# Optimization experiments

Hardware: AMD Instinct MI355X
Metric: run time of the kernel (lower is better)

Reference implementation:

```python
import jax, jax.numpy as jnp
import numpy as np

N_HEADS = 8
D_KV = 64
NUM_BUCKETS = 32
MAX_DISTANCE = 128


def _relative_position_bucket(relative_position, bidirectional=True,
                              num_buckets=NUM_BUCKETS, max_distance=MAX_DISTANCE):
    # Faithful port of T5Attention._relative_position_bucket (bidirectional path).
    n = -relative_position
    if bidirectional:
        num_buckets //= 2
        ret = (n < 0).astype(jnp.int32) * num_buckets
        n = jnp.abs(n)
    else:
        ret = jnp.zeros_like(n)
        n = jnp.maximum(n, 0)
    max_exact = num_buckets // 2
    is_small = n < max_exact
    val_if_large = max_exact + (
        jnp.log(n.astype(jnp.float32) / max_exact)
        / np.log(max_distance / max_exact)
        * (num_buckets - max_exact)
    ).astype(jnp.int32)
    val_if_large = jnp.minimum(val_if_large, num_buckets - 1)
    return ret + jnp.where(is_small, n, val_if_large)


def setup_inputs() -> dict:
    key = jax.random.key(0)
    ks = jax.random.split(key, 6)
    bs, qlen, d_model = 2, 2048, 512
    inner = N_HEADS * D_KV
    s = 1.0 / np.sqrt(d_model)
    return {
        "input": jax.random.normal(ks[0], (bs, qlen, d_model), jnp.float32),
        "Wq": jax.random.normal(ks[1], (d_model, inner), jnp.float32) * s,
        "Wk": jax.random.normal(ks[2], (d_model, inner), jnp.float32) * s,
        "Wv": jax.random.normal(ks[3], (d_model, inner), jnp.float32) * s,
        "Wo": jax.random.normal(ks[4], (inner, d_model), jnp.float32) * s,
        "rel_bias": jax.random.normal(ks[5], (NUM_BUCKETS, N_HEADS), jnp.float32),
    }


def reference(input, Wq, Wk, Wv, Wo, rel_bias):
    bs, qlen, d_model = input.shape

    def shape(x):  # [b, s, inner] -> [b, h, s, d]
        return x.reshape(bs, qlen, N_HEADS, D_KV).transpose(0, 2, 1, 3)

    q = shape(input @ Wq)
    k = shape(input @ Wk)
    v = shape(input @ Wv)

    # Raw scores (T5: no 1/sqrt(d) scaling)
    scores = jnp.einsum("bhqd,bhkd->bhqk", q, k)

    # Relative position bias: bucket [q, k] -> [h, q, k]
    pos = jnp.arange(qlen)
    rel_pos = pos[None, :] - pos[:, None]  # memory - query
    buckets = _relative_position_bucket(rel_pos, bidirectional=True)
    position_bias = rel_bias[buckets].transpose(2, 0, 1)[None]  # [1, h, q, k]

    scores = scores + position_bias
    weights = jax.nn.softmax(scores.astype(jnp.float32), axis=-1).astype(scores.dtype)

    context = jnp.einsum("bhqk,bhkd->bhqd", weights, v)
    context = context.transpose(0, 2, 1, 3).reshape(bs, qlen, N_HEADS * D_KV)
    return context @ Wo
```

## Files before the change

### kernel.cpp

```cpp
#include <hip/hip_runtime.h>
#include <hip/hip_bf16.h>
#include <cmath>

typedef __bf16 bf16_t;
typedef __bf16 bf16x8 __attribute__((ext_vector_type(8)));
typedef __bf16 bf16x4 __attribute__((ext_vector_type(4)));
typedef float f32x4 __attribute__((ext_vector_type(4)));

#define QLEN 2048
#define DMODEL 512
#define NH 8
#define DKV 64
#define INNER 512
#define LOG2E 1.44269504f
#define THR_LOG2 11.5415603f

__global__ __launch_bounds__(256) void cvt_split(const float* __restrict__ in,
                                                 bf16_t* __restrict__ hi,
                                                 bf16_t* __restrict__ lo, int n4) {
  int i = blockIdx.x * 256 + threadIdx.x;
  if (i >= n4) return;
  float4 v = reinterpret_cast<const float4*>(in)[i];
  bf16x4 h, l;
  #pragma unroll
  for (int j = 0; j < 4; ++j) {
    float x = (&v.x)[j];
    bf16_t hb = (bf16_t)x;
    h[j] = hb;
    l[j] = (bf16_t)(x - (float)hb);
  }
  reinterpret_cast<bf16x4*>(hi)[i] = h;
  reinterpret_cast<bf16x4*>(lo)[i] = l;
}

__global__ __launch_bounds__(256) void transpose512_split_all(
    const float* __restrict__ W0, const float* __restrict__ W1,
    const float* __restrict__ W2, const float* __restrict__ W3,
    bf16_t* __restrict__ H0, bf16_t* __restrict__ L0,
    bf16_t* __restrict__ H1, bf16_t* __restrict__ L1,
    bf16_t* __restrict__ H2, bf16_t* __restrict__ L2,
    bf16_t* __restrict__ H3, bf16_t* __restrict__ L3) {
  __shared__ float tile[32][33];
  int z = blockIdx.z;
  const float* W = z == 0 ? W0 : z == 1 ? W1 : z == 2 ? W2 : W3;
  bf16_t* Whi    = z == 0 ? H0 : z == 1 ? H1 : z == 2 ? H2 : H3;
  bf16_t* Wlo    = z == 0 ? L0 : z == 1 ? L1 : z == 2 ? L2 : L3;
  int bk = blockIdx.x * 32, bn = blockIdx.y * 32;
  int tx = threadIdx.x, ty = threadIdx.y;
  #pragma unroll
  for (int i = 0; i < 32; i += 8)
    tile[ty + i][tx] = W[(size_t)(bk + ty + i) * DMODEL + bn + tx];
  __syncthreads();
  #pragma unroll
  for (int i = 0; i < 32; i += 8) {
    float v = tile[tx][ty + i];
    bf16_t hb = (bf16_t)v;
    size_t o = (size_t)(bn + ty + i) * DMODEL + bk + tx;
    Whi[o] = hb;
    Wlo[o] = (bf16_t)(v - (float)hb);
  }
}

#define GST 68
template<int MODE>
__global__ __launch_bounds__(256) void gemm64(const bf16_t* __restrict__ A,
                                              const bf16_t* __restrict__ Bt,
                                              bf16_t* __restrict__ Cb,
                                              float* __restrict__ Cf) {
  __shared__ bf16_t sA[64 * GST];
  __shared__ bf16_t sB[64 * GST];
  const int m0 = blockIdx.x * 64, n0 = blockIdx.y * 64;
  const int tid = threadIdx.x;
  const int lane = tid & 63, w = tid >> 6;
  const int wr = (w >> 1) * 32, wc = (w & 1) * 32;
  const int l16 = lane & 15, lg = lane >> 4;

  f32x4 acc[2][2] = {};

  for (int k0 = 0; k0 < DMODEL; k0 += 64) {
    #pragma unroll
    for (int i = 0; i < 2; ++i) {
      int chunk = tid + i * 256;
      int row = chunk >> 3, c8 = (chunk & 7) * 8;
      *reinterpret_cast<bf16x8*>(&sA[row * GST + c8]) =
          *reinterpret_cast<const bf16x8*>(&A[(size_t)(m0 + row) * DMODEL + k0 + c8]);
      *reinterpret_cast<bf16x8*>(&sB[row * GST + c8]) =
          *reinterpret_cast<const bf16x8*>(&Bt[(size_t)(n0 + row) * DMODEL + k0 + c8]);
    }
    __syncthreads();
    #pragma unroll
    for (int ks = 0; ks < 2; ++ks) {
      bf16x8 af[2], bfr[2];
      #pragma unroll
      for (int i = 0; i < 2; ++i)
        af[i] = *reinterpret_cast<const bf16x8*>(&sA[(wr + i * 16 + l16) * GST + ks * 32 + lg * 8]);
      #pragma unroll
      for (int j = 0; j < 2; ++j)
        bfr[j] = *reinterpret_cast<const bf16x8*>(&sB[(wc + j * 16 + l16) * GST + ks * 32 + lg * 8]);
      #pragma unroll
      for (int i = 0; i < 2; ++i)
        #pragma unroll
        for (int j = 0; j < 2; ++j)
          acc[i][j] = __builtin_amdgcn_mfma_f32_16x16x32_bf16(af[i], bfr[j], acc[i][j], 0, 0, 0);
    }
    __syncthreads();
  }

  #pragma unroll
  for (int i = 0; i < 2; ++i)
    #pragma unroll
    for (int j = 0; j < 2; ++j)
      #pragma unroll
      for (int r = 0; r < 4; ++r) {
        int m = m0 + wr + i * 16 + lg * 4 + r;
        int n = n0 + wc + j * 16 + l16;
        float v = acc[i][j][r];
        if (MODE == 1) {
          int b = m >> 11, s = m & (QLEN - 1);
          Cb[(size_t)(b * INNER + n) * QLEN + s] = (bf16_t)v;
        } else {
          Cf[(size_t)m * DMODEL + n] = v;
        }
      }
}

__global__ __launch_bounds__(256) void gemm_qk_split(const bf16_t* __restrict__ Ah,
                                                     const bf16_t* __restrict__ Al,
                                                     const bf16_t* __restrict__ Bqh,
                                                     const bf16_t* __restrict__ Bql,
                                                     const bf16_t* __restrict__ Bkh,
                                                     const bf16_t* __restrict__ Bkl,
                                                     bf16_t* __restrict__ Qh,
                                                     bf16_t* __restrict__ Ql,
                                                     bf16_t* __restrict__ Kh,
                                                     bf16_t* __restrict__ Kl) {
  __shared__ bf16_t sAh[64 * GST];
  __shared__ bf16_t sAl[64 * GST];
  __shared__ bf16_t sBh[128 * GST];
  __shared__ bf16_t sBl[128 * GST];
  const int m0 = blockIdx.x * 64;
  const int n0g = blockIdx.y * 128;
  const bool isK = n0g >= 512;
  const int n0 = n0g & 511;
  const bf16_t* __restrict__ Bh = isK ? Bkh : Bqh;
  const bf16_t* __restrict__ Bl = isK ? Bkl : Bql;
  bf16_t* __restrict__ Ch = isK ? Kh : Qh;
  bf16_t* __restrict__ Cl = isK ? Kl : Ql;

  const int tid = threadIdx.x;
  const int lane = tid & 63, w = tid >> 6;
  const int wr = (w >> 1) * 32, wc = (w & 1) * 64;
  const int l16 = lane & 15, lg = lane >> 4;

  f32x4 acc[2][4] = {};

  for (int k0 = 0; k0 < DMODEL; k0 += 64) {
    #pragma unroll
    for (int i = 0; i < 2; ++i) {
      int chunk = tid + i * 256;
      int row = chunk >> 3, c8 = (chunk & 7) * 8;
      size_t ga = (size_t)(m0 + row) * DMODEL + k0 + c8;
      *reinterpret_cast<bf16x8*>(&sAh[row * GST + c8]) = *reinterpret_cast<const bf16x8*>(&Ah[ga]);
      *reinterpret_cast<bf16x8*>(&sAl[row * GST + c8]) = *reinterpret_cast<const bf16x8*>(&Al[ga]);
    }
    #pragma unroll
    for (int i = 0; i < 4; ++i) {
      int chunk = tid + i * 256;
      int row = chunk >> 3, c8 = (chunk & 7) * 8;
      size_t gb = (size_t)(n0 + row) * DMODEL + k0 + c8;
      *reinterpret_cast<bf16x8*>(&sBh[row * GST + c8]) = *reinterpret_cast<const bf16x8*>(&Bh[gb]);
      *reinterpret_cast<bf16x8*>(&sBl[row * GST + c8]) = *reinterpret_cast<const bf16x8*>(&Bl[gb]);
    }
    __syncthreads();
    #pragma unroll
    for (int ks = 0; ks < 2; ++ks) {
      bf16x8 ah[2], al[2], bh[4], bl[4];
      #pragma unroll
      for (int i = 0; i < 2; ++i) {
        int ro = (wr + i * 16 + l16) * GST + ks * 32 + lg * 8;
        ah[i] = *reinterpret_cast<const bf16x8*>(&sAh[ro]);
        al[i] = *reinterpret_cast<const bf16x8*>(&sAl[ro]);
      }
      #pragma unroll
      for (int j = 0; j < 4; ++j) {
        int ro = (wc + j * 16 + l16) * GST + ks * 32 + lg * 8;
        bh[j] = *reinterpret_cast<const bf16x8*>(&sBh[ro]);
        bl[j] = *reinterpret_cast<const bf16x8*>(&sBl[ro]);
      }
      #pragma unroll
      for (int i = 0; i < 2; ++i)
        #pragma unroll
        for (int j = 0; j < 4; ++j) {
          acc[i][j] = __builtin_amdgcn_mfma_f32_16x16x32_bf16(ah[i], bh[j], acc[i][j], 0, 0, 0);
          acc[i][j] = __builtin_amdgcn_mfma_f32_16x16x32_bf16(ah[i], bl[j], acc[i][j], 0, 0, 0);
          acc[i][j] = __builtin_amdgcn_mfma_f32_16x16x32_bf16(al[i], bh[j], acc[i][j], 0, 0, 0);
        }
    }
    __syncthreads();
  }

  #pragma unroll
  for (int i = 0; i < 2; ++i)
    #pragma unroll
    for (int j = 0; j < 4; ++j)
      #pragma unroll
      for (int r = 0; r < 4; ++r) {
        int m = m0 + wr + i * 16 + lg * 4 + r;
        int n = n0 + wc + j * 16 + l16;
        float v = acc[i][j][r];
        if (!isK) v *= LOG2E;
        bf16_t hb = (bf16_t)v;
        size_t o = (size_t)m * INNER + n;
        Ch[o] = hb;
        if (!isK) Cl[o] = (bf16_t)(v - (float)hb);
      }
}

__device__ __forceinline__ float redmax16(float v) {
  v = fmaxf(v, __shfl_xor(v, 1));
  v = fmaxf(v, __shfl_xor(v, 2));
  v = fmaxf(v, __shfl_xor(v, 4));
  v = fmaxf(v, __shfl_xor(v, 8));
  return v;
}
__device__ __forceinline__ float redsum16(float v) {
  v += __shfl_xor(v, 1);
  v += __shfl_xor(v, 2);
  v += __shfl_xor(v, 4);
  v += __shfl_xor(v, 8);
  return v;
}
__device__ __forceinline__ int t5_bucket_abs(int n) {
  if (n < 8)  return n;
  if (n < 12) return 8;
  if (n < 16) return 9;
  if (n < 23) return 10;
  if (n < 32) return 11;
  if (n < 46) return 12;
  if (n < 64) return 13;
  if (n < 91) return 14;
  return 15;
}

#define SKS 68
#define SVS 132
#define SPS 66

struct StageRegs { bf16x8 kh[2], v[2]; };

__device__ __forceinline__ void stage_load(StageRegs& r, const bf16_t* __restrict__ Kh,
                                           const bf16_t* __restrict__ Vt,
                                           int b, int h, int k0, int tid) {
  #pragma unroll
  for (int i = 0; i < 2; ++i) {
    int chunk = tid + i * 512;
    int krow = chunk >> 3, kc8 = (chunk & 7) * 8;
    int vrow = chunk >> 4, vc8 = (chunk & 15) * 8;
    r.kh[i] = *reinterpret_cast<const bf16x8*>(
        &Kh[(size_t)(b * QLEN + k0 + krow) * INNER + h * DKV + kc8]);
    r.v[i] = *reinterpret_cast<const bf16x8*>(
        &Vt[(size_t)((b * NH + h) * DKV + vrow) * QLEN + k0 + vc8]);
  }
}
__device__ __forceinline__ void stage_write(const StageRegs& r, bf16_t* dKh, bf16_t* dV,
                                            int tid) {
  #pragma unroll
  for (int i = 0; i < 2; ++i) {
    int chunk = tid + i * 512;
    int krow = chunk >> 3, kc8 = (chunk & 7) * 8;
    int vrow = chunk >> 4, vc8 = (chunk & 15) * 8;
    *reinterpret_cast<bf16x8*>(&dKh[krow * SKS + kc8]) = r.kh[i];
    *reinterpret_cast<bf16x8*>(&dV [vrow * SVS + vc8]) = r.v[i];
  }
}

__global__ __launch_bounds__(512, 4) void attn_kernel(const bf16_t* __restrict__ Qh,
                                                      const bf16_t* __restrict__ Ql,
                                                      const bf16_t* __restrict__ Kh,
                                                      const bf16_t* __restrict__ Vt,
                                                      const float* __restrict__ relb,
                                                      bf16_t* __restrict__ ctx) {
  __shared__ bf16_t sKh[128 * SKS];
  __shared__ bf16_t sV [64 * SVS];
  __shared__ bf16_t sP [2][64 * SPS];
  __shared__ float sM[2][64], sL[2][64];
  __shared__ float sBiasH[32];
  float* sAcc = (float*)&sP[0][0];

  const int id = blockIdx.x;
  const int lin = (id & 7) * 64 + (id >> 3);
  const int qt = lin & 31, h = (lin >> 5) & 7, b = lin >> 8;

  const int tid = threadIdx.x, lane = tid & 63, w = tid >> 6;
  const int l16 = lane & 15, lg = lane >> 4;
  const int q0 = qt * 64;
  const int qg = w & 3, half = w >> 2;
  const int wq = qg * 16;
  const int kh0 = half * 64;

  if (tid < 32) sBiasH[tid] = relb[tid * NH + h] * LOG2E;

  bf16x8 qh[2], ql[2];
  #pragma unroll
  for (int ks = 0; ks < 2; ++ks) {
    size_t o = (size_t)(b * QLEN + q0 + wq + l16) * INNER + h * DKV + ks * 32 + lg * 8;
    qh[ks] = *reinterpret_cast<const bf16x8*>(&Qh[o]);
    ql[ks] = *reinterpret_cast<const bf16x8*>(&Ql[o]);
  }

  f32x4 acc[4] = {};
  float mrow[4], lpart[4];
  #pragma unroll
  for (int r = 0; r < 4; ++r) { mrow[r] = -INFINITY; lpart[r] = 0.f; }

  const int NT = QLEN / 128;
  StageRegs sreg;
  stage_load(sreg, Kh, Vt, b, h, 0, tid);
  stage_write(sreg, sKh, sV, tid);
  __syncthreads();

  for (int kt = 0; kt < NT; ++kt) {
    const int k0 = kt * 128;
    const bool pf = (kt + 1 < NT);
    if (pf) stage_load(sreg, Kh, Vt, b, h, k0 + 128, tid);

    f32x4 s[4] = {};
    __builtin_amdgcn_s_setprio(1);
    #pragma unroll
    for (int ks = 0; ks < 2; ++ks) {
      bf16x8 kf[4];
      #pragma unroll
      for (int ni = 0; ni < 4; ++ni)
        kf[ni] = *reinterpret_cast<const bf16x8*>(
            &sKh[(kh0 + ni * 16 + l16) * SKS + ks * 32 + lg * 8]);
      #pragma unroll
      for (int ni = 0; ni < 4; ++ni) {
        s[ni] = __builtin_amdgcn_mfma_f32_16x16x32_bf16(qh[ks], kf[ni], s[ni], 0, 0, 0);
        s[ni] = __builtin_amdgcn_mfma_f32_16x16x32_bf16(ql[ks], kf[ni], s[ni], 0, 0, 0);
      }
    }
    __builtin_amdgcn_s_setprio(0);

    const int kbase = k0 + kh0;
    const int dmin = q0 - (kbase + 63);
    const int dmax = q0 + 63 - kbase;
    const bool farP = dmin >= 91, farN = dmax <= -91;
    float fbias = 0.f;
    if (farP) fbias = sBiasH[15];
    else if (farN) fbias = sBiasH[31];
    else {
      #pragma unroll
      for (int ni = 0; ni < 4; ++ni) {
        int kcol = kbase + ni * 16 + l16;
        #pragma unroll
        for (int r = 0; r < 4; ++r) {
          int qrow = q0 + wq + lg * 4 + r;
          int d = qrow - kcol;
          int n = d < 0 ? -d : d;
          int bk = t5_bucket_abs(n) + (d < 0 ? 16 : 0);
          s[ni][r] += sBiasH[bk];
        }
      }
    }

    float c[4], tmx[4];
    #pragma unroll
    for (int r = 0; r < 4; ++r) {
      tmx[r] = fmaxf(fmaxf(s[0][r], s[1][r]), fmaxf(s[2][r], s[3][r]));
      c[r] = mrow[r] - fbias;
    }
    float u = fmaxf(fmaxf(tmx[0] - c[0], tmx[1] - c[1]), fmaxf(tmx[2] - c[2], tmx[3] - c[3]));
    if (__any(u > THR_LOG2)) {
      #pragma unroll
      for (int r = 0; r < 4; ++r) {
        float rm = redmax16(tmx[r]) + fbias;
        float mnew = fmaxf(mrow[r], rm);
        float alpha = exp2f(mrow[r] - mnew);
        mrow[r] = mnew;
        c[r] = mnew - fbias;
        lpart[r] *= alpha;
        #pragma unroll
        for (int di = 0; di < 4; ++di) acc[di][r] *= alpha;
      }
    }

    #pragma unroll
    for (int r = 0; r < 4; ++r) {
      float ps = 0.f;
      #pragma unroll
      for (int ni = 0; ni < 4; ++ni) {
        float p = exp2f(s[ni][r] - c[r]);
        ps += p;
        sP[half][(wq + lg * 4 + r) * SPS + ni * 16 + l16] = (bf16_t)p;
      }
      lpart[r] += ps;
    }

    __builtin_amdgcn_s_setprio(1);
    #pragma unroll
    for (int ks = 0; ks < 2; ++ks) {
      bf16x8 pfr, vf[4];
      pfr = *reinterpret_cast<const bf16x8*>(&sP[half][(wq + l16) * SPS + ks * 32 + lg * 8]);
      #pragma unroll
      for (int di = 0; di < 4; ++di)
        vf[di] = *reinterpret_cast<const bf16x8*>(
            &sV[(di * 16 + l16) * SVS + kh0 + ks * 32 + lg * 8]);
      #pragma unroll
      for (int di = 0; di < 4; ++di)
        acc[di] = __builtin_amdgcn_mfma_f32_16x16x32_bf16(pfr, vf[di], acc[di], 0, 0, 0);
    }
    __builtin_amdgcn_s_setprio(0);

    __syncthreads();
    if (pf) stage_write(sreg, sKh, sV, tid);
    __syncthreads();
  }

  float lrow[4];
  #pragma unroll
  for (int r = 0; r < 4; ++r) lrow[r] = redsum16(lpart[r]);

  if (l16 == 0) {
    #pragma unroll
    for (int r = 0; r < 4; ++r) {
      int row = wq + lg * 4 + r;
      sM[half][row] = mrow[r];
      sL[half][row] = lrow[r];
    }
  }
  __syncthreads();

  float eh[4], denom[4];
  #pragma unroll
  for (int r = 0; r < 4; ++r) {
    int row = wq + lg * 4 + r;
    float m0 = sM[0][row], m1 = sM[1][row];
    float l0 = sL[0][row], l1 = sL[1][row];
    float M = fmaxf(m0, m1);
    float e0 = exp2f(m0 - M), e1 = exp2f(m1 - M);
    denom[r] = l0 * e0 + l1 * e1;
    eh[r] = half ? e1 : e0;
  }

  if (half == 1) {
    #pragma unroll
    for (int di = 0; di < 4; ++di)
      #pragma unroll
      for (int r = 0; r < 4; ++r)
        sAcc[(wq + lg * 4 + r) * SPS + di * 16 + l16] = acc[di][r] * eh[r];
  }
  __syncthreads();

  if (half == 0) {
    #pragma unroll
    for (int di = 0; di < 4; ++di)
      #pragma unroll
      for (int r = 0; r < 4; ++r) {
        int row = wq + lg * 4 + r;
        float v = (acc[di][r] * eh[r] + sAcc[row * SPS + di * 16 + l16]) / denom[r];
        ctx[(size_t)(b * QLEN + q0 + row) * INNER + h * DKV + di * 16 + l16] = (bf16_t)v;
      }
  }
}

extern "C" void kernel_launch(void* const* d_in, const int* in_sizes, int n_in,
                              void* d_out, int out_size, void* d_ws, size_t ws_size,
                              hipStream_t stream) {
  const float* X    = (const float*)d_in[0];
  const float* Wq   = (const float*)d_in[1];
  const float* Wk   = (const float*)d_in[2];
  const float* Wv   = (const float*)d_in[3];
  const float* Wo   = (const float*)d_in[4];
  const float* relb = (const float*)d_in[5];
  float* out = (float*)d_out;

  const size_t WSZ = 262144, XSZ = 2097152;
  bf16_t* ws   = (bf16_t*)d_ws;
  bf16_t* Wq_h = ws;              bf16_t* Wq_l = Wq_h + WSZ;
  bf16_t* Wk_h = Wq_l + WSZ;      bf16_t* Wk_l = Wk_h + WSZ;
  bf16_t* Wv_h = Wk_l + WSZ;      bf16_t* Wv_l = Wv_h + WSZ;
  bf16_t* Wo_h = Wv_l + WSZ;      bf16_t* Wo_l = Wo_h + WSZ;
  bf16_t* Xh   = Wo_l + WSZ;      bf16_t* Xl   = Xh + XSZ;
  bf16_t* Q_h  = Xl + XSZ;        bf16_t* Q_l  = Q_h + XSZ;
  bf16_t* K_h  = Q_l + XSZ;       bf16_t* K_l  = K_h + XSZ;
  bf16_t* Vt   = Xl;
  bf16_t* ctx  = Xh;

  transpose512_split_all<<<dim3(16, 16, 4), dim3(32, 8), 0, stream>>>(
      Wq, Wk, Wv, Wo, Wq_h, Wq_l, Wk_h, Wk_l, Wv_h, Wv_l, Wo_h, Wo_l);

  int n4 = (2 * QLEN * DMODEL) / 4;
  cvt_split<<<n4 / 256, 256, 0, stream>>>(X, Xh, Xl, n4);

  gemm_qk_split<<<dim3(64, 8), 256, 0, stream>>>(Xh, Xl, Wq_h, Wq_l, Wk_h, Wk_l,
                                                 Q_h, Q_l, K_h, K_l);
  gemm64<1><<<dim3(64, 8), 256, 0, stream>>>(Xh, Wv_h, Vt, nullptr);

  attn_kernel<<<dim3(512), 512, 0, stream>>>(Q_h, Q_l, K_h, Vt, relb, ctx);

  gemm64<2><<<dim3(64, 8), 256, 0, stream>>>(ctx, Wo_h, nullptr, out);
}
```

Before: 119.7 us.

## Split attention over key halves, add merge kernel, swizzle LDS layouts

```diff
diff --git a/kernel.cpp b/kernel.cpp
--- a/kernel.cpp
+++ b/kernel.cpp
@@ -61,7 +61,7 @@
   }
 }
 
-#define GST 68
+#define GST 72
 template<int MODE>
 __global__ __launch_bounds__(256) void gemm64(const bf16_t* __restrict__ A,
                                               const bf16_t* __restrict__ Bt,
@@ -242,9 +242,7 @@
   return 15;
 }
 
-#define SKS 68
-#define SVS 132
-#define SPS 66
+#define HALFELEMS 2097152
 
 struct StageRegs { bf16x8 kh[2], v[2]; };
 
@@ -262,15 +260,15 @@
         &Vt[(size_t)((b * NH + h) * DKV + vrow) * QLEN + k0 + vc8]);
   }
 }
-__device__ __forceinline__ void stage_write(const StageRegs& r, bf16_t* dKh, bf16_t* dV,
+__device__ __forceinline__ void stage_write(const StageRegs& r, bf16_t* dK, bf16_t* dV,
                                             int tid) {
   #pragma unroll
   for (int i = 0; i < 2; ++i) {
     int chunk = tid + i * 512;
     int krow = chunk >> 3, kc8 = (chunk & 7) * 8;
     int vrow = chunk >> 4, vc8 = (chunk & 15) * 8;
-    *reinterpret_cast<bf16x8*>(&dKh[krow * SKS + kc8]) = r.kh[i];
-    *reinterpret_cast<bf16x8*>(&dV [vrow * SVS + vc8]) = r.v[i];
+    *reinterpret_cast<bf16x8*>(&dK[krow * 64 + (kc8 ^ ((krow & 7) << 3))]) = r.kh[i];
+    *reinterpret_cast<bf16x8*>(&dV[vrow * 128 + (vc8 ^ ((vrow & 7) << 3))]) = r.v[i];
   }
 }
 
@@ -279,17 +277,18 @@
                                                       const bf16_t* __restrict__ Kh,
                                                       const bf16_t* __restrict__ Vt,
                                                       const float* __restrict__ relb,
-                                                      bf16_t* __restrict__ ctx) {
-  __shared__ bf16_t sKh[128 * SKS];
-  __shared__ bf16_t sV [64 * SVS];
-  __shared__ bf16_t sP [2][64 * SPS];
+                                                      bf16_t* __restrict__ pPart,
+                                                      float* __restrict__ pMl) {
+  __shared__ bf16_t sKh[128 * 64];
+  __shared__ bf16_t sV [64 * 128];
+  __shared__ bf16_t sP [2][64 * 64];
   __shared__ float sM[2][64], sL[2][64];
   __shared__ float sBiasH[32];
   float* sAcc = (float*)&sP[0][0];
 
   const int id = blockIdx.x;
-  const int lin = (id & 7) * 64 + (id >> 3);
-  const int qt = lin & 31, h = (lin >> 5) & 7, b = lin >> 8;
+  const int lin = (id & 7) * 128 + (id >> 3);
+  const int qt = lin & 31, h = (lin >> 5) & 7, b = (lin >> 8) & 1, sp = lin >> 9;
 
   const int tid = threadIdx.x, lane = tid & 63, w = tid >> 6;
   const int l16 = lane & 15, lg = lane >> 4;
@@ -313,15 +312,16 @@
   #pragma unroll
   for (int r = 0; r < 4; ++r) { mrow[r] = -INFINITY; lpart[r] = 0.f; }
 
-  const int NT = QLEN / 128;
+  const int NT = 8;
+  const int ktBase = sp * 8;
   StageRegs sreg;
-  stage_load(sreg, Kh, Vt, b, h, 0, tid);
+  stage_load(sreg, Kh, Vt, b, h, ktBase * 128, tid);
   stage_write(sreg, sKh, sV, tid);
   __syncthreads();
 
-  for (int kt = 0; kt < NT; ++kt) {
-    const int k0 = kt * 128;
-    const bool pf = (kt + 1 < NT);
+  for (int it = 0; it < NT; ++it) {
+    const int k0 = (ktBase + it) * 128;
+    const bool pf = (it + 1 < NT);
     if (pf) stage_load(sreg, Kh, Vt, b, h, k0 + 128, tid);
 
     f32x4 s[4] = {};
@@ -330,9 +330,11 @@
     for (int ks = 0; ks < 2; ++ks) {
       bf16x8 kf[4];
       #pragma unroll
-      for (int ni = 0; ni < 4; ++ni)
-        kf[ni] = *reinterpret_cast<const bf16x8*>(
-            &sKh[(kh0 + ni * 16 + l16) * SKS + ks * 32 + lg * 8]);
+      for (int ni = 0; ni < 4; ++ni) {
+        int row = kh0 + ni * 16 + l16;
+        int col = (ks * 32 + lg * 8) ^ ((row & 7) << 3);
+        kf[ni] = *reinterpret_cast<const bf16x8*>(&sKh[row * 64 + col]);
+      }
       #pragma unroll
       for (int ni = 0; ni < 4; ++ni) {
         s[ni] = __builtin_amdgcn_mfma_f32_16x16x32_bf16(qh[ks], kf[ni], s[ni], 0, 0, 0);
@@ -387,11 +389,13 @@
     #pragma unroll
     for (int r = 0; r < 4; ++r) {
       float ps = 0.f;
+      int prow = wq + lg * 4 + r;
+      int psw = (prow & 7) << 3;
       #pragma unroll
       for (int ni = 0; ni < 4; ++ni) {
         float p = exp2f(s[ni][r] - c[r]);
         ps += p;
-        sP[half][(wq + lg * 4 + r) * SPS + ni * 16 + l16] = (bf16_t)p;
+        sP[half][prow * 64 + ((ni * 16 + l16) ^ psw)] = (bf16_t)p;
       }
       lpart[r] += ps;
     }
@@ -399,12 +403,16 @@
     __builtin_amdgcn_s_setprio(1);
     #pragma unroll
     for (int ks = 0; ks < 2; ++ks) {
-      bf16x8 pfr, vf[4];
-      pfr = *reinterpret_cast<const bf16x8*>(&sP[half][(wq + l16) * SPS + ks * 32 + lg * 8]);
-      #pragma unroll
-      for (int di = 0; di < 4; ++di)
-        vf[di] = *reinterpret_cast<const bf16x8*>(
-            &sV[(di * 16 + l16) * SVS + kh0 + ks * 32 + lg * 8]);
+      int prow = wq + l16;
+      bf16x8 pfr = *reinterpret_cast<const bf16x8*>(
+          &sP[half][prow * 64 + ((ks * 32 + lg * 8) ^ ((prow & 7) << 3))]);
+      bf16x8 vf[4];
+      #pragma unroll
+      for (int di = 0; di < 4; ++di) {
+        int vrow = di * 16 + l16;
+        int vcol = (kh0 + ks * 32 + lg * 8) ^ ((vrow & 7) << 3);
+        vf[di] = *reinterpret_cast<const bf16x8*>(&sV[vrow * 128 + vcol]);
+      }
       #pragma unroll
       for (int di = 0; di < 4; ++di)
         acc[di] = __builtin_amdgcn_mfma_f32_16x16x32_bf16(pfr, vf[di], acc[di], 0, 0, 0);
@@ -430,7 +438,7 @@
   }
   __syncthreads();
 
-  float eh[4], denom[4];
+  float eh[4], denom[4], Mc[4];
   #pragma unroll
   for (int r = 0; r < 4; ++r) {
     int row = wq + lg * 4 + r;
@@ -440,6 +448,7 @@
     float e0 = exp2f(m0 - M), e1 = exp2f(m1 - M);
     denom[r] = l0 * e0 + l1 * e1;
     eh[r] = half ? e1 : e0;
+    Mc[r] = M;
   }
 
   if (half == 1) {
@@ -447,20 +456,51 @@
     for (int di = 0; di < 4; ++di)
       #pragma unroll
       for (int r = 0; r < 4; ++r)
-        sAcc[(wq + lg * 4 + r) * SPS + di * 16 + l16] = acc[di][r] * eh[r];
+        sAcc[(wq + lg * 4 + r) * 64 + di * 16 + l16] = acc[di][r] * eh[r];
   }
   __syncthreads();
 
   if (half == 0) {
+    const int rowbase = (b * NH + h) * QLEN + q0 + wq;
     #pragma unroll
     for (int di = 0; di < 4; ++di)
       #pragma unroll
       for (int r = 0; r < 4; ++r) {
-        int row = wq + lg * 4 + r;
-        float v = (acc[di][r] * eh[r] + sAcc[row * SPS + di * 16 + l16]) / denom[r];
-        ctx[(size_t)(b * QLEN + q0 + row) * INNER + h * DKV + di * 16 + l16] = (bf16_t)v;
-      }
-  }
+        int rl = wq + lg * 4 + r;
+        float v = (acc[di][r] * eh[r] + sAcc[rl * 64 + di * 16 + l16]) / denom[r];
+        pPart[(size_t)sp * HALFELEMS + (size_t)(rowbase + lg * 4 + r) * 64 + di * 16 + l16] =
+            (bf16_t)v;
+      }
+    if (l16 == 0) {
+      #pragma unroll
+      for (int r = 0; r < 4; ++r) {
+        int row = rowbase + lg * 4 + r;
+        float2 v; v.x = Mc[r]; v.y = denom[r];
+        *reinterpret_cast<float2*>(&pMl[sp * 65536 + row * 2]) = v;
+      }
+    }
+  }
+}
+
+__global__ __launch_bounds__(256) void attn_merge(const bf16_t* __restrict__ pPart,
+                                                  const float* __restrict__ pMl,
+                                                  bf16_t* __restrict__ ctx) {
+  int idx = blockIdx.x * 256 + threadIdx.x;
+  int row = idx >> 3, d8 = (idx & 7) * 8;
+  bf16x8 p0 = *reinterpret_cast<const bf16x8*>(&pPart[(size_t)row * 64 + d8]);
+  bf16x8 p1 = *reinterpret_cast<const bf16x8*>(&pPart[HALFELEMS + (size_t)row * 64 + d8]);
+  float2 ml0 = *reinterpret_cast<const float2*>(&pMl[row * 2]);
+  float2 ml1 = *reinterpret_cast<const float2*>(&pMl[65536 + row * 2]);
+  float M = fmaxf(ml0.x, ml1.x);
+  float w0 = ml0.y * exp2f(ml0.x - M), w1 = ml1.y * exp2f(ml1.x - M);
+  float inv = 1.f / (w0 + w1);
+  w0 *= inv; w1 *= inv;
+  int b = row >> 14, h = (row >> 11) & 7, q = row & 2047;
+  bf16x8 o;
+  #pragma unroll
+  for (int j = 0; j < 8; ++j)
+    o[j] = (bf16_t)((float)p0[j] * w0 + (float)p1[j] * w1);
+  *reinterpret_cast<bf16x8*>(&ctx[((size_t)(b * QLEN + q)) * INNER + h * DKV + d8]) = o;
 }
 
 extern "C" void kernel_launch(void* const* d_in, const int* in_sizes, int n_in,
@@ -485,6 +525,8 @@
   bf16_t* K_h  = Q_l + XSZ;       bf16_t* K_l  = K_h + XSZ;
   bf16_t* Vt   = Xl;
   bf16_t* ctx  = Xh;
+  bf16_t* pPart = (bf16_t*)d_out;
+  float*  pMl   = (float*)Wq_h;
 
   transpose512_split_all<<<dim3(16, 16, 4), dim3(32, 8), 0, stream>>>(
       Wq, Wk, Wv, Wo, Wq_h, Wq_l, Wk_h, Wk_l, Wv_h, Wv_l, Wo_h, Wo_l);
@@ -496,7 +538,8 @@
                                                  Q_h, Q_l, K_h, K_l);
   gemm64<1><<<dim3(64, 8), 256, 0, stream>>>(Xh, Wv_h, Vt, nullptr);
 
-  attn_kernel<<<dim3(512), 512, 0, stream>>>(Q_h, Q_l, K_h, Vt, relb, ctx);
+  attn_kernel<<<dim3(1024), 512, 0, stream>>>(Q_h, Q_l, K_h, Vt, relb, pPart, pMl);
+  attn_merge<<<dim3(1024), 256, 0, stream>>>(pPart, pMl, ctx);
 
   gemm64<2><<<dim3(64, 8), 256, 0, stream>>>(ctx, Wo_h, nullptr, out);
 }
```

Result: slower. 128.9 us (+7.7%).
